# Optimization experiments

Measured on AMD Instinct MI355X. Metric: run time of the kernel, lower is better.

Reference implementation:

```python
import jax, jax.numpy as jnp
import numpy as np

LATENT = 128
N_NODES = 50000
N_EDGES = 800000
LN_EPS = 1e-5


def _glorot(key, fan_in, fan_out):
    lim = np.sqrt(6.0 / (fan_in + fan_out)).astype(np.float32)
    return jax.random.uniform(key, (fan_in, fan_out), jnp.float32, -lim, lim)


def setup_inputs() -> dict:
    key = jax.random.key(0)
    ks = jax.random.split(key, 10)
    node_latents = jax.random.normal(ks[0], (1, N_NODES, LATENT), jnp.float32)
    mesh_edge_latents = jax.random.normal(ks[1], (1, N_EDGES, LATENT), jnp.float32)
    senders = jax.random.randint(ks[2], (N_EDGES,), 0, N_NODES, jnp.int32)
    receivers = jax.random.randint(ks[3], (N_EDGES,), 0, N_NODES, jnp.int32)
    # mesh_edge_net: Linear(3L, L), ReLU, Linear(L, L), ReLU, LayerNorm(L)
    me_w1 = _glorot(ks[4], 3 * LATENT, LATENT)
    me_b1 = jnp.zeros((LATENT,), jnp.float32)
    me_w2 = _glorot(ks[5], LATENT, LATENT)
    me_b2 = jnp.zeros((LATENT,), jnp.float32)
    me_g = jnp.ones((LATENT,), jnp.float32)
    me_beta = jnp.zeros((LATENT,), jnp.float32)
    # node_feature_net: Linear(2L, L), ReLU, Linear(L, L), ReLU, LayerNorm(L)
    nf_w1 = _glorot(ks[6], 2 * LATENT, LATENT)
    nf_b1 = jnp.zeros((LATENT,), jnp.float32)
    nf_w2 = _glorot(ks[7], LATENT, LATENT)
    nf_b2 = jnp.zeros((LATENT,), jnp.float32)
    nf_g = jnp.ones((LATENT,), jnp.float32)
    nf_beta = jnp.zeros((LATENT,), jnp.float32)
    return dict(node_latents=node_latents, mesh_edge_latents=mesh_edge_latents,
                senders=senders, receivers=receivers,
                me_w1=me_w1, me_b1=me_b1, me_w2=me_w2, me_b2=me_b2, me_g=me_g, me_beta=me_beta,
                nf_w1=nf_w1, nf_b1=nf_b1, nf_w2=nf_w2, nf_b2=nf_b2, nf_g=nf_g, nf_beta=nf_beta)


def _mlp_ln(x, w1, b1, w2, b2, g, beta):
    h = jax.nn.relu(x @ w1 + b1)
    h = jax.nn.relu(h @ w2 + b2)
    mu = jnp.mean(h, axis=-1, keepdims=True)
    var = jnp.var(h, axis=-1, keepdims=True)
    return (h - mu) * jax.lax.rsqrt(var + LN_EPS) * g + beta


def reference(node_latents, mesh_edge_latents, senders, receivers,
              me_w1, me_b1, me_w2, me_b2, me_g, me_beta,
              nf_w1, nf_b1, nf_w2, nf_b2, nf_g, nf_beta):
    # gather sender/receiver node features: [B, E, L]
    edge_in = jnp.concatenate([node_latents[:, senders, :],
                               node_latents[:, receivers, :],
                               mesh_edge_latents], axis=-1)
    new_edges = _mlp_ln(edge_in, me_w1, me_b1, me_w2, me_b2, me_g, me_beta)
    # scatter_add messages to receiver nodes along dim=1
    aggr = jax.vmap(lambda e: jax.ops.segment_sum(e, receivers, num_segments=N_NODES))(new_edges)
    node_in = jnp.concatenate([node_latents, aggr], axis=-1)
    new_nodes = _mlp_ln(node_in, nf_w1, nf_b1, nf_w2, nf_b2, nf_g, nf_beta)
    new_nodes = new_nodes + node_latents  # residual
    new_edges = new_edges + mesh_edge_latents  # residual
    return new_nodes, new_edges
```

## Files before the change

kernel.cpp:

```cpp
#include <hip/hip_runtime.h>
#include <stdint.h>

typedef unsigned short u16;
typedef __bf16 bf16x8 __attribute__((ext_vector_type(8)));
typedef float f32x4 __attribute__((ext_vector_type(4)));

#define N_NODES 50000
#define N_EDGES 800000
#define LN_EPS 1e-5f

__device__ __forceinline__ uint4 pack8(const float* __restrict__ p) {
    const float4 f0 = ((const float4*)p)[0];
    const float4 f1 = ((const float4*)p)[1];
    union { __bf16 b[8]; uint4 q; } t;
    t.b[0] = (__bf16)f0.x; t.b[1] = (__bf16)f0.y; t.b[2] = (__bf16)f0.z; t.b[3] = (__bf16)f0.w;
    t.b[4] = (__bf16)f1.x; t.b[5] = (__bf16)f1.y; t.b[6] = (__bf16)f1.z; t.b[7] = (__bf16)f1.w;
    return t.q;
}

__global__ void pack_weights(const float* __restrict__ w1e, const float* __restrict__ w2e,
                             const float* __restrict__ w1n, const float* __restrict__ w2n,
                             uint4* __restrict__ out)
{
    const int t = blockIdx.x * 256 + threadIdx.x;
    const float* W; int idx;
    if (t < 6144)       { W = w1e; idx = t; }
    else if (t < 8192)  { W = w2e; idx = t - 6144; }
    else if (t < 12288) { W = w1n; idx = t - 8192; }
    else                { W = w2n; idx = t - 12288; }
    const int lane = idx & 63;
    const int col16 = (idx >> 6) & 7;
    const int kb = idx >> 9;
    const int row0 = kb * 32 + (lane >> 4) * 8;
    const int col = col16 * 16 + (lane & 15);
    union { __bf16 b[8]; uint4 q; } v;
#pragma unroll
    for (int j = 0; j < 8; ++j) v.b[j] = (__bf16)W[(size_t)(row0 + j) * 128 + col];
    out[t] = v.q;
}

__global__ __launch_bounds__(256, 3)
void edge_mlp_kernel(const float* __restrict__ node, const float* __restrict__ elat,
                     const int* __restrict__ senders, const int* __restrict__ receivers,
                     const float* __restrict__ b1, const float* __restrict__ b2,
                     const float* __restrict__ gam, const float* __restrict__ bet,
                     const uint4* __restrict__ w1p, const uint4* __restrict__ w2p,
                     float* __restrict__ eout, float* __restrict__ aggr)
{
    __shared__ __align__(16) u16 x_lds[3 * 64 * 128];
    __shared__ int rcv_s[64];

    float2* part = (float2*)(x_lds + 8192);
    float*  muv  = (float*)(x_lds + 8192 + 1024);
    float*  rsv  = (float*)(x_lds + 8192 + 1152);

    const int tid = threadIdx.x;
    const int w = tid >> 6;
    const int lane = tid & 63;
    const int cl = lane & 15;
    const int q = lane >> 4;
    const int n_base = w * 32;

    float b1v[2], b2v[2], gv[2], bv[2];
#pragma unroll
    for (int n = 0; n < 2; ++n) {
        const int c = n_base + n * 16 + cl;
        b1v[n] = b1[c]; b2v[n] = b2[c];
        gv[n]  = gam[c]; bv[n] = bet[c];
    }

    for (int tile = blockIdx.x; tile < N_EDGES / 64; tile += gridDim.x) {
        const int base = tile * 64;

        {
            const int ch = tid & 15;
            const int r0 = tid >> 4;
#pragma unroll
            for (int gp = 0; gp < 4; ++gp) {
                const int row = gp * 16 + r0;
                const int rx = row & 7;
                const int sn = senders[base + row];
                const int rc = receivers[base + row];
                if (ch == 0) rcv_s[row] = rc;
                uint4* dst = (uint4*)x_lds + row * 16;
                dst[ch ^ rx]          = pack8(node + (size_t)sn * 128 + ch * 8);
                dst[1024 + (ch ^ rx)] = pack8(node + (size_t)rc * 128 + ch * 8);
                dst[2048 + (ch ^ rx)] = pack8(elat + (size_t)(base + row) * 128 + ch * 8);
            }
        }
        __syncthreads();

        f32x4 acc[4][2];
#pragma unroll
        for (int m = 0; m < 4; ++m)
#pragma unroll
            for (int n = 0; n < 2; ++n)
#pragma unroll
                for (int r = 0; r < 4; ++r) acc[m][n][r] = 0.f;

        uint4 wreg[14][2];
#pragma unroll
        for (int kb = 0; kb < 2; ++kb)
#pragma unroll
            for (int n = 0; n < 2; ++n)
                wreg[kb][n] = w1p[(kb * 8 + w * 2 + n) * 64 + lane];

#pragma unroll
        for (int kb = 0; kb < 12; ++kb) {
            if (kb + 2 < 12) {
#pragma unroll
                for (int n = 0; n < 2; ++n)
                    wreg[kb + 2][n] = w1p[((kb + 2) * 8 + w * 2 + n) * 64 + lane];
            }
            const int p = kb >> 2, k2 = kb & 3;
            bf16x8 a[4];
#pragma unroll
            for (int m = 0; m < 4; ++m) {
                const int row = m * 16 + cl;
                a[m] = __builtin_bit_cast(bf16x8,
                    ((const uint4*)x_lds)[p * 1024 + row * 16 + ((k2 * 4 + q) ^ (row & 7))]);
            }
#pragma unroll
            for (int m = 0; m < 4; ++m)
#pragma unroll
                for (int n = 0; n < 2; ++n)
                    acc[m][n] = __builtin_amdgcn_mfma_f32_16x16x32_bf16(
                        a[m], __builtin_bit_cast(bf16x8, wreg[kb][n]), acc[m][n], 0, 0, 0);
        }

        uint4 w2reg[4][2];
#pragma unroll
        for (int kb = 0; kb < 4; ++kb)
#pragma unroll
            for (int n = 0; n < 2; ++n)
                w2reg[kb][n] = w2p[(kb * 8 + w * 2 + n) * 64 + lane];

        __syncthreads();

        {
            __bf16* hb = (__bf16*)x_lds;
#pragma unroll
            for (int m = 0; m < 4; ++m)
#pragma unroll
                for (int n = 0; n < 2; ++n)
#pragma unroll
                    for (int r = 0; r < 4; ++r) {
                        const int row = m * 16 + q * 4 + r;
                        const int col = n_base + n * 16 + cl;
                        hb[row * 128 + (((col >> 3) ^ (row & 7)) << 3) + (col & 7)] =
                            (__bf16)fmaxf(acc[m][n][r] + b1v[n], 0.f);
                    }
        }
        __syncthreads();

#pragma unroll
        for (int m = 0; m < 4; ++m)
#pragma unroll
            for (int n = 0; n < 2; ++n)
#pragma unroll
                for (int r = 0; r < 4; ++r) acc[m][n][r] = 0.f;
#pragma unroll
        for (int kb = 0; kb < 4; ++kb) {
            bf16x8 a[4];
#pragma unroll
            for (int m = 0; m < 4; ++m) {
                const int row = m * 16 + cl;
                a[m] = __builtin_bit_cast(bf16x8,
                    ((const uint4*)x_lds)[row * 16 + ((kb * 4 + q) ^ (row & 7))]);
            }
#pragma unroll
            for (int m = 0; m < 4; ++m)
#pragma unroll
                for (int n = 0; n < 2; ++n)
                    acc[m][n] = __builtin_amdgcn_mfma_f32_16x16x32_bf16(
                        a[m], __builtin_bit_cast(bf16x8, w2reg[kb][n]), acc[m][n], 0, 0, 0);
        }

#pragma unroll
        for (int m = 0; m < 4; ++m)
#pragma unroll
            for (int n = 0; n < 2; ++n)
#pragma unroll
                for (int r = 0; r < 4; ++r)
                    acc[m][n][r] = fmaxf(acc[m][n][r] + b2v[n], 0.f);

#pragma unroll
        for (int m = 0; m < 4; ++m)
#pragma unroll
            for (int r = 0; r < 4; ++r) {
                float s  = acc[m][0][r] + acc[m][1][r];
                float ss = acc[m][0][r] * acc[m][0][r] + acc[m][1][r] * acc[m][1][r];
#pragma unroll
                for (int off = 1; off < 16; off <<= 1) {
                    s  += __shfl_xor(s, off, 64);
                    ss += __shfl_xor(ss, off, 64);
                }
                if (cl == 0) part[w * 64 + m * 16 + q * 4 + r] = make_float2(s, ss);
            }
        __syncthreads();
        if (tid < 64) {
            float s = 0.f, ss = 0.f;
#pragma unroll
            for (int ww = 0; ww < 4; ++ww) { const float2 pp = part[ww * 64 + tid]; s += pp.x; ss += pp.y; }
            const float mu = s * (1.f / 128.f);
            const float var = ss * (1.f / 128.f) - mu * mu;
            muv[tid] = mu;
            rsv[tid] = rsqrtf(var + LN_EPS);
        }
        __syncthreads();

#pragma unroll
        for (int m = 0; m < 4; ++m)
#pragma unroll
            for (int r = 0; r < 4; ++r) {
                const int row = m * 16 + q * 4 + r;
                const float mu = muv[row];
                const float rs = rsv[row];
                const int rc = rcv_s[row];
                float* orow = eout + (size_t)(base + row) * 128;
#pragma unroll
                for (int n = 0; n < 2; ++n) {
                    const int col = n_base + n * 16 + cl;
                    const float ln = (acc[m][n][r] - mu) * rs * gv[n] + bv[n];
                    atomicAdd(&aggr[(size_t)rc * 128 + col], ln);
                    const float e = (float)((__bf16*)x_lds)[16384 + row * 128 + (((col >> 3) ^ (row & 7)) << 3) + (col & 7)];
                    orow[col] = ln + e;
                }
            }
        __syncthreads();
    }
}

__global__ __launch_bounds__(256, 4)
void node_mlp_kernel(const float* __restrict__ node, const float* __restrict__ aggr,
                     const float* __restrict__ b1, const float* __restrict__ b2,
                     const float* __restrict__ gam, const float* __restrict__ bet,
                     const uint4* __restrict__ w1p, const uint4* __restrict__ w2p,
                     float* __restrict__ nout)
{
    __shared__ __align__(16) u16 x_lds[2 * 64 * 128];
    __shared__ float2 part[256];
    __shared__ float muv[64], rsv[64];

    const int tid = threadIdx.x;
    const int w = tid >> 6;
    const int lane = tid & 63;
    const int cl = lane & 15;
    const int q = lane >> 4;
    const int n_base = w * 32;

    float b1v[2], b2v[2], gv[2], bv[2];
#pragma unroll
    for (int n = 0; n < 2; ++n) {
        const int c = n_base + n * 16 + cl;
        b1v[n] = b1[c]; b2v[n] = b2[c];
        gv[n]  = gam[c]; bv[n] = bet[c];
    }

    const int ntiles = (N_NODES + 63) / 64;
    for (int tile = blockIdx.x; tile < ntiles; tile += gridDim.x) {
        const int base = tile * 64;

        {
            const int ch = tid & 15;
            const int r0 = tid >> 4;
#pragma unroll
            for (int gp = 0; gp < 4; ++gp) {
                const int row = gp * 16 + r0;
                const int rx = row & 7;
                int gn = base + row;
                if (gn >= N_NODES) gn = N_NODES - 1;
                uint4* dst = (uint4*)x_lds + row * 16;
                dst[ch ^ rx]          = pack8(node + (size_t)gn * 128 + ch * 8);
                dst[1024 + (ch ^ rx)] = pack8(aggr + (size_t)gn * 128 + ch * 8);
            }
        }
        __syncthreads();

        f32x4 acc[4][2];
#pragma unroll
        for (int m = 0; m < 4; ++m)
#pragma unroll
            for (int n = 0; n < 2; ++n)
#pragma unroll
                for (int r = 0; r < 4; ++r) acc[m][n][r] = 0.f;

        uint4 wreg[10][2];
#pragma unroll
        for (int kb = 0; kb < 2; ++kb)
#pragma unroll
            for (int n = 0; n < 2; ++n)
                wreg[kb][n] = w1p[(kb * 8 + w * 2 + n) * 64 + lane];

#pragma unroll
        for (int kb = 0; kb < 8; ++kb) {
            if (kb + 2 < 8) {
#pragma unroll
                for (int n = 0; n < 2; ++n)
                    wreg[kb + 2][n] = w1p[((kb + 2) * 8 + w * 2 + n) * 64 + lane];
            }
            const int p = kb >> 2, k2 = kb & 3;
            bf16x8 a[4];
#pragma unroll
            for (int m = 0; m < 4; ++m) {
                const int row = m * 16 + cl;
                a[m] = __builtin_bit_cast(bf16x8,
                    ((const uint4*)x_lds)[p * 1024 + row * 16 + ((k2 * 4 + q) ^ (row & 7))]);
            }
#pragma unroll
            for (int m = 0; m < 4; ++m)
#pragma unroll
                for (int n = 0; n < 2; ++n)
                    acc[m][n] = __builtin_amdgcn_mfma_f32_16x16x32_bf16(
                        a[m], __builtin_bit_cast(bf16x8, wreg[kb][n]), acc[m][n], 0, 0, 0);
        }

        uint4 w2reg[4][2];
#pragma unroll
        for (int kb = 0; kb < 4; ++kb)
#pragma unroll
            for (int n = 0; n < 2; ++n)
                w2reg[kb][n] = w2p[(kb * 8 + w * 2 + n) * 64 + lane];

        __syncthreads();

        {
            __bf16* hb = (__bf16*)(x_lds + 8192);
#pragma unroll
            for (int m = 0; m < 4; ++m)
#pragma unroll
                for (int n = 0; n < 2; ++n)
#pragma unroll
                    for (int r = 0; r < 4; ++r) {
                        const int row = m * 16 + q * 4 + r;
                        const int col = n_base + n * 16 + cl;
                        hb[row * 128 + (((col >> 3) ^ (row & 7)) << 3) + (col & 7)] =
                            (__bf16)fmaxf(acc[m][n][r] + b1v[n], 0.f);
                    }
        }
        __syncthreads();

#pragma unroll
        for (int m = 0; m < 4; ++m)
#pragma unroll
            for (int n = 0; n < 2; ++n)
#pragma unroll
                for (int r = 0; r < 4; ++r) acc[m][n][r] = 0.f;
#pragma unroll
        for (int kb = 0; kb < 4; ++kb) {
            bf16x8 a[4];
#pragma unroll
            for (int m = 0; m < 4; ++m) {
                const int row = m * 16 + cl;
                a[m] = __builtin_bit_cast(bf16x8,
                    ((const uint4*)x_lds)[1024 + row * 16 + ((kb * 4 + q) ^ (row & 7))]);
            }
#pragma unroll
            for (int m = 0; m < 4; ++m)
#pragma unroll
                for (int n = 0; n < 2; ++n)
                    acc[m][n] = __builtin_amdgcn_mfma_f32_16x16x32_bf16(
                        a[m], __builtin_bit_cast(bf16x8, w2reg[kb][n]), acc[m][n], 0, 0, 0);
        }
#pragma unroll
        for (int m = 0; m < 4; ++m)
#pragma unroll
            for (int n = 0; n < 2; ++n)
#pragma unroll
                for (int r = 0; r < 4; ++r)
                    acc[m][n][r] = fmaxf(acc[m][n][r] + b2v[n], 0.f);

#pragma unroll
        for (int m = 0; m < 4; ++m)
#pragma unroll
            for (int r = 0; r < 4; ++r) {
                float s  = acc[m][0][r] + acc[m][1][r];
                float ss = acc[m][0][r] * acc[m][0][r] + acc[m][1][r] * acc[m][1][r];
#pragma unroll
                for (int off = 1; off < 16; off <<= 1) {
                    s  += __shfl_xor(s, off, 64);
                    ss += __shfl_xor(ss, off, 64);
                }
                if (cl == 0) part[w * 64 + m * 16 + q * 4 + r] = make_float2(s, ss);
            }
        __syncthreads();
        if (tid < 64) {
            float s = 0.f, ss = 0.f;
#pragma unroll
            for (int ww = 0; ww < 4; ++ww) { const float2 pp = part[ww * 64 + tid]; s += pp.x; ss += pp.y; }
            const float mu = s * (1.f / 128.f);
            const float var = ss * (1.f / 128.f) - mu * mu;
            muv[tid] = mu;
            rsv[tid] = rsqrtf(var + LN_EPS);
        }
        __syncthreads();

#pragma unroll
        for (int m = 0; m < 4; ++m)
#pragma unroll
            for (int r = 0; r < 4; ++r) {
                const int row = m * 16 + q * 4 + r;
                if (base + row < N_NODES) {
                    const float mu = muv[row];
                    const float rs = rsv[row];
                    float* orow = nout + (size_t)(base + row) * 128;
#pragma unroll
                    for (int n = 0; n < 2; ++n) {
                        const int col = n_base + n * 16 + cl;
                        const float ln = (acc[m][n][r] - mu) * rs * gv[n] + bv[n];
                        const float e = (float)((__bf16*)x_lds)[row * 128 + (((col >> 3) ^ (row & 7)) << 3) + (col & 7)];
                        orow[col] = ln + e;
                    }
                }
            }
        __syncthreads();
    }
}

extern "C" void kernel_launch(void* const* d_in, const int* in_sizes, int n_in,
                              void* d_out, int out_size, void* d_ws, size_t ws_size,
                              hipStream_t stream) {
    (void)in_sizes; (void)n_in; (void)out_size;
    const float* node = (const float*)d_in[0];
    const float* elat = (const float*)d_in[1];
    const int* senders = (const int*)d_in[2];
    const int* receivers = (const int*)d_in[3];
    const float* me_w1 = (const float*)d_in[4];
    const float* me_b1 = (const float*)d_in[5];
    const float* me_w2 = (const float*)d_in[6];
    const float* me_b2 = (const float*)d_in[7];
    const float* me_g  = (const float*)d_in[8];
    const float* me_be = (const float*)d_in[9];
    const float* nf_w1 = (const float*)d_in[10];
    const float* nf_b1 = (const float*)d_in[11];
    const float* nf_w2 = (const float*)d_in[12];
    const float* nf_b2 = (const float*)d_in[13];
    const float* nf_g  = (const float*)d_in[14];
    const float* nf_be = (const float*)d_in[15];

    float* out_nodes = (float*)d_out;
    float* out_edges = out_nodes + (size_t)N_NODES * 128;
    float* aggr = (float*)d_ws;
    const size_t aggr_bytes = (size_t)N_NODES * 128 * sizeof(float);
    uint4* wpack = (uint4*)((char*)d_ws + aggr_bytes);
    if (ws_size < aggr_bytes + 14336 * sizeof(uint4)) return;

    hipMemsetAsync(aggr, 0, aggr_bytes, stream);
    pack_weights<<<56, 256, 0, stream>>>(me_w1, me_w2, nf_w1, nf_w2, wpack);
    edge_mlp_kernel<<<768, 256, 0, stream>>>(node, elat, senders, receivers,
                                             me_b1, me_b2, me_g, me_be,
                                             wpack, wpack + 6144,
                                             out_edges, aggr);
    node_mlp_kernel<<<782, 256, 0, stream>>>(node, aggr,
                                             nf_b1, nf_b2, nf_g, nf_be,
                                             wpack + 8192, wpack + 12288,
                                             out_nodes);
}
```

Baseline: 1.009 ms.

## Sort edges by receiver and segment-reduce messages before scattering to aggregate

Builds a counting sort of edges by receiver (histogram, single-block scan, atomic scatter) and has the edge MLP process tiles in receiver-sorted order. Each tile's LayerNorm outputs are staged in LDS and reduced over runs of equal receivers per column, so there is one write per receiver run instead of one atomicAdd per edge element. Interior runs use plain stores and boundary runs use atomics. The cost is three extra small kernels, a serial one-block scan, and scattered writes of edge outputs and gathers of edge latents by sorted id.

```diff
diff --git a/kernel.cpp b/kernel.cpp
--- a/kernel.cpp
+++ b/kernel.cpp
@@ -39,9 +39,49 @@
     out[t] = v.q;
 }
 
+__global__ void hist_kernel(const int* __restrict__ receivers, int* __restrict__ cnt) {
+    const int e = blockIdx.x * 256 + threadIdx.x;
+    if (e < N_EDGES) atomicAdd(&cnt[receivers[e]], 1);
+}
+
+__global__ void scan_kernel(const int* __restrict__ cnt, int* __restrict__ cursor) {
+    __shared__ int sums[1024];
+    const int t = threadIdx.x;
+    const int CH = 49;
+    const int base = t * CH;
+    int s = 0;
+#pragma unroll 1
+    for (int i = 0; i < CH; ++i) { const int idx = base + i; if (idx < N_NODES) s += cnt[idx]; }
+    sums[t] = s;
+    __syncthreads();
+    for (int off = 1; off < 1024; off <<= 1) {
+        const int v = (t >= off) ? sums[t - off] : 0;
+        __syncthreads();
+        sums[t] += v;
+        __syncthreads();
+    }
+    int run = sums[t] - s;
+#pragma unroll 1
+    for (int i = 0; i < CH; ++i) {
+        const int idx = base + i;
+        if (idx < N_NODES) { cursor[idx] = run; run += cnt[idx]; }
+    }
+}
+
+__global__ void scatter_kernel(const int* __restrict__ receivers, int* __restrict__ cursor,
+                               int* __restrict__ sorted_eid) {
+    const int e = blockIdx.x * 256 + threadIdx.x;
+    if (e < N_EDGES) {
+        const int pos = atomicAdd(&cursor[receivers[e]], 1);
+        sorted_eid[pos] = e;
+    }
+}
+
+template<int SORTED>
 __global__ __launch_bounds__(256, 3)
 void edge_mlp_kernel(const float* __restrict__ node, const float* __restrict__ elat,
                      const int* __restrict__ senders, const int* __restrict__ receivers,
+                     const int* __restrict__ sorted_eid,
                      const float* __restrict__ b1, const float* __restrict__ b2,
                      const float* __restrict__ gam, const float* __restrict__ bet,
                      const uint4* __restrict__ w1p, const uint4* __restrict__ w2p,
@@ -49,10 +89,11 @@
 {
     __shared__ __align__(16) u16 x_lds[3 * 64 * 128];
     __shared__ int rcv_s[64];
-
-    float2* part = (float2*)(x_lds + 8192);
-    float*  muv  = (float*)(x_lds + 8192 + 1024);
-    float*  rsv  = (float*)(x_lds + 8192 + 1152);
+    __shared__ int eid_s[64];
+    __shared__ float2 part[256];
+    __shared__ float muv[64], rsv[64];
+
+    float* lnf = (float*)x_lds;
 
     const int tid = threadIdx.x;
     const int w = tid >> 6;
@@ -79,13 +120,14 @@
             for (int gp = 0; gp < 4; ++gp) {
                 const int row = gp * 16 + r0;
                 const int rx = row & 7;
-                const int sn = senders[base + row];
-                const int rc = receivers[base + row];
-                if (ch == 0) rcv_s[row] = rc;
+                const int eid = SORTED ? sorted_eid[base + row] : (base + row);
+                const int sn = senders[eid];
+                const int rc = receivers[eid];
+                if (ch == 0) { rcv_s[row] = rc; eid_s[row] = eid; }
                 uint4* dst = (uint4*)x_lds + row * 16;
                 dst[ch ^ rx]          = pack8(node + (size_t)sn * 128 + ch * 8);
                 dst[1024 + (ch ^ rx)] = pack8(node + (size_t)rc * 128 + ch * 8);
-                dst[2048 + (ch ^ rx)] = pack8(elat + (size_t)(base + row) * 128 + ch * 8);
+                dst[2048 + (ch ^ rx)] = pack8(elat + (size_t)eid * 128 + ch * 8);
             }
         }
         __syncthreads();
@@ -216,17 +258,39 @@
                 const int row = m * 16 + q * 4 + r;
                 const float mu = muv[row];
                 const float rs = rsv[row];
-                const int rc = rcv_s[row];
-                float* orow = eout + (size_t)(base + row) * 128;
+                float* orow = eout + (size_t)eid_s[row] * 128;
 #pragma unroll
                 for (int n = 0; n < 2; ++n) {
                     const int col = n_base + n * 16 + cl;
                     const float ln = (acc[m][n][r] - mu) * rs * gv[n] + bv[n];
-                    atomicAdd(&aggr[(size_t)rc * 128 + col], ln);
+                    lnf[row * 128 + col] = ln;
                     const float e = (float)((__bf16*)x_lds)[16384 + row * 128 + (((col >> 3) ^ (row & 7)) << 3) + (col & 7)];
                     orow[col] = ln + e;
                 }
             }
+        __syncthreads();
+
+        {
+            const int c = tid & 127;
+            const int h = tid >> 7;
+            const int rstart = h * 32, rend = rstart + 32;
+            float sacc = 0.f; int flushed = 0;
+#pragma unroll 1
+            for (int r = rstart; r < rend; ++r) {
+                sacc += lnf[r * 128 + c];
+                const int rc = rcv_s[r];
+                const bool last = (r == 63);
+                const bool bnd = last || (rc != rcv_s[r + 1]);
+                if (bnd) {
+                    float* dst = &aggr[(size_t)rc * 128 + c];
+                    if (SORTED && !last && flushed) *dst = sacc;
+                    else atomicAdd(dst, sacc);
+                    sacc = 0.f; flushed = 1;
+                }
+            }
+            if (sacc != 0.f)
+                atomicAdd(&aggr[(size_t)rcv_s[rend - 1] * 128 + c], sacc);
+        }
         __syncthreads();
     }
 }
@@ -440,17 +504,42 @@
 
     float* out_nodes = (float*)d_out;
     float* out_edges = out_nodes + (size_t)N_NODES * 128;
-    float* aggr = (float*)d_ws;
-    const size_t aggr_bytes = (size_t)N_NODES * 128 * sizeof(float);
-    uint4* wpack = (uint4*)((char*)d_ws + aggr_bytes);
-    if (ws_size < aggr_bytes + 14336 * sizeof(uint4)) return;
-
-    hipMemsetAsync(aggr, 0, aggr_bytes, stream);
+
+    char* ws = (char*)d_ws;
+    const size_t off_aggr   = 0;
+    const size_t off_wpack  = off_aggr  + (size_t)N_NODES * 128 * sizeof(float);
+    const size_t off_cnt    = off_wpack + 14336 * sizeof(uint4);
+    const size_t off_cursor = off_cnt   + (size_t)N_NODES * sizeof(int);
+    const size_t off_sorted = off_cursor+ (size_t)N_NODES * sizeof(int);
+    const size_t need_full  = off_sorted+ (size_t)N_EDGES * sizeof(int);
+    const size_t need_min   = off_cnt;
+    if (ws_size < need_min) return;
+
+    float* aggr   = (float*)(ws + off_aggr);
+    uint4* wpack  = (uint4*)(ws + off_wpack);
+    int*   cnt    = (int*)(ws + off_cnt);
+    int*   cursor = (int*)(ws + off_cursor);
+    int*   sorted = (int*)(ws + off_sorted);
+    const bool use_sort = (ws_size >= need_full);
+
+    hipMemsetAsync(aggr, 0, (size_t)N_NODES * 128 * sizeof(float), stream);
     pack_weights<<<56, 256, 0, stream>>>(me_w1, me_w2, nf_w1, nf_w2, wpack);
-    edge_mlp_kernel<<<768, 256, 0, stream>>>(node, elat, senders, receivers,
-                                             me_b1, me_b2, me_g, me_be,
-                                             wpack, wpack + 6144,
-                                             out_edges, aggr);
+
+    if (use_sort) {
+        hipMemsetAsync(cnt, 0, (size_t)N_NODES * sizeof(int), stream);
+        hist_kernel<<<(N_EDGES + 255) / 256, 256, 0, stream>>>(receivers, cnt);
+        scan_kernel<<<1, 1024, 0, stream>>>(cnt, cursor);
+        scatter_kernel<<<(N_EDGES + 255) / 256, 256, 0, stream>>>(receivers, cursor, sorted);
+        edge_mlp_kernel<1><<<768, 256, 0, stream>>>(node, elat, senders, receivers, sorted,
+                                                    me_b1, me_b2, me_g, me_be,
+                                                    wpack, wpack + 6144,
+                                                    out_edges, aggr);
+    } else {
+        edge_mlp_kernel<0><<<768, 256, 0, stream>>>(node, elat, senders, receivers, nullptr,
+                                                    me_b1, me_b2, me_g, me_be,
+                                                    wpack, wpack + 6144,
+                                                    out_edges, aggr);
+    }
     node_mlp_kernel<<<782, 256, 0, stream>>>(node, aggr,
                                              nf_b1, nf_b2, nf_g, nf_be,
                                              wpack + 8192, wpack + 12288,
```

Result: slower. 1.162 ms (+15.2%).

## Pre-convert node and edge latents to bf16 and prefetch next edge tile

Applied to the files above, without the earlier changes.

Node latents are converted to bf16 once up front, stored temporarily in the node output buffer, and edge latents are converted into workspace when it is large enough. The edge kernel then gathers half-width rows and software-pipelines the gather by loading the next tile's indices and rows into registers while the current tile computes. The aim is to cut gather traffic and hide global-memory latency. The cost is extra conversion passes (the edge-latent pass reads and writes a large array), higher register pressure from the prefetch buffers, and relying on the output buffer as scratch before the node kernel overwrites it.

```diff
diff --git a/kernel.cpp b/kernel.cpp
--- a/kernel.cpp
+++ b/kernel.cpp
@@ -7,6 +7,7 @@
 
 #define N_NODES 50000
 #define N_EDGES 800000
+#define NTILES  (N_EDGES / 64)
 #define LN_EPS 1e-5f
 
 __device__ __forceinline__ uint4 pack8(const float* __restrict__ p) {
@@ -39,20 +40,29 @@
     out[t] = v.q;
 }
 
+__global__ void convert_node(const float* __restrict__ node, uint4* __restrict__ node_bf) {
+    const int idx = blockIdx.x * 256 + threadIdx.x;
+    node_bf[idx] = pack8(node + (size_t)idx * 8);
+}
+__global__ void convert_elat(const float* __restrict__ elat, uint4* __restrict__ elat_bf) {
+    const int idx = blockIdx.x * 256 + threadIdx.x;
+    elat_bf[idx] = pack8(elat + (size_t)idx * 8);
+}
+
+template<int EBF>
 __global__ __launch_bounds__(256, 3)
-void edge_mlp_kernel(const float* __restrict__ node, const float* __restrict__ elat,
-                     const int* __restrict__ senders, const int* __restrict__ receivers,
-                     const float* __restrict__ b1, const float* __restrict__ b2,
-                     const float* __restrict__ gam, const float* __restrict__ bet,
-                     const uint4* __restrict__ w1p, const uint4* __restrict__ w2p,
-                     float* __restrict__ eout, float* __restrict__ aggr)
+void edge_pipe(const u16* __restrict__ node_bf,
+               const float* __restrict__ elat32, const u16* __restrict__ elat_bf,
+               const int* __restrict__ senders, const int* __restrict__ receivers,
+               const float* __restrict__ b1, const float* __restrict__ b2,
+               const float* __restrict__ gam, const float* __restrict__ bet,
+               const uint4* __restrict__ w1p, const uint4* __restrict__ w2p,
+               float* __restrict__ eout, float* __restrict__ aggr)
 {
     __shared__ __align__(16) u16 x_lds[3 * 64 * 128];
     __shared__ int rcv_s[64];
-
-    float2* part = (float2*)(x_lds + 8192);
-    float*  muv  = (float*)(x_lds + 8192 + 1024);
-    float*  rsv  = (float*)(x_lds + 8192 + 1152);
+    __shared__ float2 part[256];
+    __shared__ float muv[64], rsv[64];
 
     const int tid = threadIdx.x;
     const int w = tid >> 6;
@@ -60,6 +70,8 @@
     const int cl = lane & 15;
     const int q = lane >> 4;
     const int n_base = w * 32;
+    const int ch = tid & 15;
+    const int r0 = tid >> 4;
 
     float b1v[2], b2v[2], gv[2], bv[2];
 #pragma unroll
@@ -69,26 +81,72 @@
         gv[n]  = gam[c]; bv[n] = bet[c];
     }
 
-    for (int tile = blockIdx.x; tile < N_EDGES / 64; tile += gridDim.x) {
+    const int stride = gridDim.x;
+
+    int sn_nxt[4], rc_nxt[4], rc_cur[4];
+    uint4 pf_s[4], pf_r[4], pf_e[4];
+
+    {
+        const int tb = blockIdx.x * 64;
+#pragma unroll
+        for (int gp = 0; gp < 4; ++gp) {
+            sn_nxt[gp] = senders[tb + gp * 16 + r0];
+            rc_nxt[gp] = receivers[tb + gp * 16 + r0];
+        }
+#pragma unroll
+        for (int gp = 0; gp < 4; ++gp) {
+            pf_s[gp] = ((const uint4*)(node_bf + (size_t)sn_nxt[gp] * 128))[ch];
+            pf_r[gp] = ((const uint4*)(node_bf + (size_t)rc_nxt[gp] * 128))[ch];
+            if (EBF)
+                pf_e[gp] = ((const uint4*)(elat_bf + (size_t)(tb + gp * 16 + r0) * 128))[ch];
+            rc_cur[gp] = rc_nxt[gp];
+        }
+        int t1 = blockIdx.x + stride; if (t1 >= NTILES) t1 = blockIdx.x;
+        const int tb1 = t1 * 64;
+#pragma unroll
+        for (int gp = 0; gp < 4; ++gp) {
+            sn_nxt[gp] = senders[tb1 + gp * 16 + r0];
+            rc_nxt[gp] = receivers[tb1 + gp * 16 + r0];
+        }
+    }
+
+    for (int tile = blockIdx.x; tile < NTILES; tile += stride) {
         const int base = tile * 64;
 
+#pragma unroll
+        for (int gp = 0; gp < 4; ++gp) {
+            const int row = gp * 16 + r0;
+            const int rx = row & 7;
+            uint4* dst = (uint4*)x_lds + row * 16;
+            dst[ch ^ rx]          = pf_s[gp];
+            dst[1024 + (ch ^ rx)] = pf_r[gp];
+            if (EBF) dst[2048 + (ch ^ rx)] = pf_e[gp];
+            else     dst[2048 + (ch ^ rx)] = pack8(elat32 + (size_t)(base + gp * 16 + r0) * 128 + ch * 8);
+            if (ch == 0) rcv_s[row] = rc_cur[gp];
+        }
+        __syncthreads();
+
         {
-            const int ch = tid & 15;
-            const int r0 = tid >> 4;
-#pragma unroll
-            for (int gp = 0; gp < 4; ++gp) {
-                const int row = gp * 16 + r0;
-                const int rx = row & 7;
-                const int sn = senders[base + row];
-                const int rc = receivers[base + row];
-                if (ch == 0) rcv_s[row] = rc;
-                uint4* dst = (uint4*)x_lds + row * 16;
-                dst[ch ^ rx]          = pack8(node + (size_t)sn * 128 + ch * 8);
-                dst[1024 + (ch ^ rx)] = pack8(node + (size_t)rc * 128 + ch * 8);
-                dst[2048 + (ch ^ rx)] = pack8(elat + (size_t)(base + row) * 128 + ch * 8);
-            }
-        }
-        __syncthreads();
+            const int tn = tile + stride;
+            if (tn < NTILES) {
+                const int tb = tn * 64;
+#pragma unroll
+                for (int gp = 0; gp < 4; ++gp) {
+                    pf_s[gp] = ((const uint4*)(node_bf + (size_t)sn_nxt[gp] * 128))[ch];
+                    pf_r[gp] = ((const uint4*)(node_bf + (size_t)rc_nxt[gp] * 128))[ch];
+                    if (EBF)
+                        pf_e[gp] = ((const uint4*)(elat_bf + (size_t)(tb + gp * 16 + r0) * 128))[ch];
+                    rc_cur[gp] = rc_nxt[gp];
+                }
+                int tnn = tn + stride; if (tnn >= NTILES) tnn = tn;
+                const int tb2 = tnn * 64;
+#pragma unroll
+                for (int gp = 0; gp < 4; ++gp) {
+                    sn_nxt[gp] = senders[tb2 + gp * 16 + r0];
+                    rc_nxt[gp] = receivers[tb2 + gp * 16 + r0];
+                }
+            }
+        }
 
         f32x4 acc[4][2];
 #pragma unroll
@@ -260,7 +318,6 @@
     const int ntiles = (N_NODES + 63) / 64;
     for (int tile = blockIdx.x; tile < ntiles; tile += gridDim.x) {
         const int base = tile * 64;
-
         {
             const int ch = tid & 15;
             const int r0 = tid >> 4;
@@ -284,14 +341,12 @@
             for (int n = 0; n < 2; ++n)
 #pragma unroll
                 for (int r = 0; r < 4; ++r) acc[m][n][r] = 0.f;
-
         uint4 wreg[10][2];
 #pragma unroll
         for (int kb = 0; kb < 2; ++kb)
 #pragma unroll
             for (int n = 0; n < 2; ++n)
                 wreg[kb][n] = w1p[(kb * 8 + w * 2 + n) * 64 + lane];
-
 #pragma unroll
         for (int kb = 0; kb < 8; ++kb) {
             if (kb + 2 < 8) {
@@ -314,16 +369,13 @@
                     acc[m][n] = __builtin_amdgcn_mfma_f32_16x16x32_bf16(
                         a[m], __builtin_bit_cast(bf16x8, wreg[kb][n]), acc[m][n], 0, 0, 0);
         }
-
         uint4 w2reg[4][2];
 #pragma unroll
         for (int kb = 0; kb < 4; ++kb)
 #pragma unroll
             for (int n = 0; n < 2; ++n)
                 w2reg[kb][n] = w2p[(kb * 8 + w * 2 + n) * 64 + lane];
-
-        __syncthreads();
-
+        __syncthreads();
         {
             __bf16* hb = (__bf16*)(x_lds + 8192);
 #pragma unroll
@@ -339,7 +391,6 @@
                     }
         }
         __syncthreads();
-
 #pragma unroll
         for (int m = 0; m < 4; ++m)
 #pragma unroll
@@ -369,7 +420,6 @@
 #pragma unroll
                 for (int r = 0; r < 4; ++r)
                     acc[m][n][r] = fmaxf(acc[m][n][r] + b2v[n], 0.f);
-
 #pragma unroll
         for (int m = 0; m < 4; ++m)
 #pragma unroll
@@ -394,7 +444,6 @@
             rsv[tid] = rsqrtf(var + LN_EPS);
         }
         __syncthreads();
-
 #pragma unroll
         for (int m = 0; m < 4; ++m)
 #pragma unroll
@@ -440,17 +489,38 @@
 
     float* out_nodes = (float*)d_out;
     float* out_edges = out_nodes + (size_t)N_NODES * 128;
-    float* aggr = (float*)d_ws;
-    const size_t aggr_bytes = (size_t)N_NODES * 128 * sizeof(float);
-    uint4* wpack = (uint4*)((char*)d_ws + aggr_bytes);
-    if (ws_size < aggr_bytes + 14336 * sizeof(uint4)) return;
-
-    hipMemsetAsync(aggr, 0, aggr_bytes, stream);
+
+    u16* node_bf = (u16*)d_out;
+
+    char* ws = (char*)d_ws;
+    const size_t off_aggr   = 0;
+    const size_t off_wpack  = off_aggr  + (size_t)N_NODES * 128 * sizeof(float);
+    const size_t off_elat   = off_wpack + 14336 * sizeof(uint4);
+    const size_t need_min   = off_elat;
+    const size_t need_ebf   = off_elat + (size_t)N_EDGES * 128 * sizeof(u16);
+    if (ws_size < need_min) return;
+
+    float* aggr    = (float*)(ws + off_aggr);
+    uint4* wpack   = (uint4*)(ws + off_wpack);
+    u16*   elat_bf = (u16*)(ws + off_elat);
+    const bool ebf = (ws_size >= need_ebf);
+
+    hipMemsetAsync(aggr, 0, (size_t)N_NODES * 128 * sizeof(float), stream);
     pack_weights<<<56, 256, 0, stream>>>(me_w1, me_w2, nf_w1, nf_w2, wpack);
-    edge_mlp_kernel<<<768, 256, 0, stream>>>(node, elat, senders, receivers,
-                                             me_b1, me_b2, me_g, me_be,
-                                             wpack, wpack + 6144,
-                                             out_edges, aggr);
+    convert_node<<<3125, 256, 0, stream>>>(node, (uint4*)node_bf);
+
+    if (ebf) {
+        convert_elat<<<50000, 256, 0, stream>>>(elat, (uint4*)elat_bf);
+        edge_pipe<1><<<768, 256, 0, stream>>>(node_bf, elat, elat_bf, senders, receivers,
+                                              me_b1, me_b2, me_g, me_be,
+                                              wpack, wpack + 6144,
+                                              out_edges, aggr);
+    } else {
+        edge_pipe<0><<<768, 256, 0, stream>>>(node_bf, elat, elat_bf, senders, receivers,
+                                              me_b1, me_b2, me_g, me_be,
+                                              wpack, wpack + 6144,
+                                              out_edges, aggr);
+    }
     node_mlp_kernel<<<782, 256, 0, stream>>>(node, aggr,
                                              nf_b1, nf_b2, nf_g, nf_be,
                                              wpack + 8192, wpack + 12288,
```

After: 1.639 ms. +62.5%, slower.
